# Optimization experiments

Hardware: AMD Instinct MI355X
Metric: run time of the kernel (lower is better)

## Reference

```python
import jax, jax.numpy as jnp
import numpy as np

EMBED_DIM = 1024
NUM_HEADS = 16
HEAD_DIM = EMBED_DIM // NUM_HEADS
INV_SQRT_DIM = 1.0 / np.sqrt(EMBED_DIM).astype(np.float32)  # note: embed_dim, not head_dim


def setup_inputs() -> dict:
    key = jax.random.key(0)
    k1, k2 = jax.random.split(key)
    hidden_states = jax.random.normal(k1, (2, 2048, EMBED_DIM), dtype=jnp.float32)
    # nn.Linear(embed_dim, 3*embed_dim, bias=False); store as [in, out] so y = x @ w_qkv
    w_qkv = jax.random.normal(k2, (EMBED_DIM, 3 * EMBED_DIM), dtype=jnp.float32) * 0.02
    return {"hidden_states": hidden_states, "w_qkv": w_qkv}


def reference(hidden_states, w_qkv):
    b, s, _ = hidden_states.shape
    qkv = hidden_states @ w_qkv  # [b, s, 3*E]
    q, k, v = jnp.split(qkv, 3, axis=-1)

    def split_heads(x):  # [b, s, E] -> [b, h, s, d]
        return x.reshape(b, s, NUM_HEADS, HEAD_DIM).transpose(0, 2, 1, 3)

    q, k, v = split_heads(q), split_heads(k), split_heads(v)
    scores = jnp.einsum('bhqd,bhkd->bhqk', q, k) * INV_SQRT_DIM
    w = jax.nn.softmax(scores, axis=-1)
    out = jnp.einsum('bhqk,bhkd->bhqd', w, v)  # [b, h, s, d]
    return out.transpose(0, 2, 1, 3).reshape(b, s, EMBED_DIM)
```

## Files before the change

### kernel.cpp

```cpp
#include <hip/hip_runtime.h>
#include <stdint.h>


typedef __attribute__((ext_vector_type(8))) short v8s;
typedef __attribute__((ext_vector_type(4))) float v4f;

__device__ __forceinline__ unsigned short bf16bits(float f) {
  union { float f; unsigned int u; } c; c.f = f;
  unsigned int u = c.u;
  unsigned int r = (u + 0x7fffu + ((u >> 16) & 1u)) >> 16;
  return (unsigned short)r;
}

__device__ __forceinline__ v4f mfma16(v8s a, v8s b, v4f c) {
  return __builtin_amdgcn_mfma_f32_16x16x32_bf16(a, b, c, 0, 0, 0);
}

#define GLD16(g, l) __builtin_amdgcn_global_load_lds( \
    (const __attribute__((address_space(1))) unsigned int*)(g), \
    (__attribute__((address_space(3))) unsigned int*)(l), 16, 0, 0)

__global__ __launch_bounds__(256) void cvt_x_kernel(const float4* __restrict__ x4,
                                                    ushort4* __restrict__ o4, int n4) {
  int i = blockIdx.x * 256 + threadIdx.x;
  if (i < n4) {
    float4 v = x4[i];
    ushort4 o;
    o.x = bf16bits(v.x); o.y = bf16bits(v.y); o.z = bf16bits(v.z); o.w = bf16bits(v.w);
    o4[i] = o;
  }
}

__global__ __launch_bounds__(256) void cvt_wT_kernel(const float* __restrict__ w,
                                                     unsigned short* __restrict__ wt) {
  __shared__ float t[32][33];
  int n0 = blockIdx.x * 32, k0 = blockIdx.y * 32;
  int tx = threadIdx.x & 31, ty = threadIdx.x >> 5;
  for (int i = 0; i < 4; ++i) {
    int kr = ty + i * 8;
    t[kr][tx] = w[(k0 + kr) * 3072 + n0 + tx];
  }
  __syncthreads();
  for (int i = 0; i < 4; ++i) {
    int nr = ty + i * 8;
    wt[(n0 + nr) * 1024 + k0 + tx] = bf16bits(t[tx][nr]);
  }
}

__global__ __launch_bounds__(256) void qkv_gemm(const unsigned short* __restrict__ A,
                                                const unsigned short* __restrict__ Bm,
                                                unsigned short* __restrict__ Qh,
                                                unsigned short* __restrict__ Kh,
                                                unsigned short* __restrict__ VTh) {
  __shared__ __align__(16) unsigned short As[128 * 64];
  __shared__ __align__(16) unsigned short Bs[128 * 64];
  int bm = blockIdx.x, bn = blockIdx.y;
  int tid = threadIdx.x, lane = tid & 63, wave = tid >> 6;
  int wr = wave >> 1, wc = wave & 1;

  v4f acc[4][4];
  for (int i = 0; i < 4; ++i)
    for (int j = 0; j < 4; ++j) acc[i][j] = (v4f){0.f, 0.f, 0.f, 0.f};

  for (int kk = 0; kk < 1024; kk += 64) {
    __syncthreads();
    for (int i = 0; i < 4; ++i) {
      int e = i * 256 + tid;
      int row = e >> 3, cc = e & 7;
      int sc = cc ^ (row & 7);
      GLD16(A + (bm * 128 + row) * 1024 + kk + sc * 8,
            (char*)As + (i * 256 + wave * 64) * 16);
    }
    for (int i = 0; i < 4; ++i) {
      int e = i * 256 + tid;
      int row = e >> 3, cc = e & 7;
      int sc = cc ^ (row & 7);
      GLD16(Bm + (bn * 128 + row) * 1024 + kk + sc * 8,
            (char*)Bs + (i * 256 + wave * 64) * 16);
    }
    __syncthreads();
    for (int ks = 0; ks < 2; ++ks) {
      v8s af[4], bf[4];
      for (int rt = 0; rt < 4; ++rt) {
        int ra = wr * 64 + rt * 16 + (lane & 15);
        int ca = (ks * 4 + (lane >> 4)) ^ (ra & 7);
        af[rt] = *(const v8s*)&As[ra * 64 + ca * 8];
      }
      for (int ct = 0; ct < 4; ++ct) {
        int rb = wc * 64 + ct * 16 + (lane & 15);
        int cb = (ks * 4 + (lane >> 4)) ^ (rb & 7);
        bf[ct] = *(const v8s*)&Bs[rb * 64 + cb * 8];
      }
      for (int rt = 0; rt < 4; ++rt)
        for (int ct = 0; ct < 4; ++ct)
          acc[rt][ct] = mfma16(af[rt], bf[ct], acc[rt][ct]);
    }
  }

  int which = (bn * 128) >> 10;
  for (int ct = 0; ct < 4; ++ct) {
    int n = bn * 128 + wc * 64 + ct * 16 + (lane & 15);
    int rem = n & 1023, head = rem >> 6, d = rem & 63;
    for (int rt = 0; rt < 4; ++rt) {
      int m = bm * 128 + wr * 64 + rt * 16 + ((lane >> 4) << 2);
      int b = m >> 11, s = m & 2047;
      int bh = b * 16 + head;
      if (which == 2) {
        ushort4 pk;
        pk.x = bf16bits(acc[rt][ct][0]); pk.y = bf16bits(acc[rt][ct][1]);
        pk.z = bf16bits(acc[rt][ct][2]); pk.w = bf16bits(acc[rt][ct][3]);
        *(ushort4*)&VTh[(bh * 64 + d) * 2048 + s] = pk;
      } else {
        unsigned short* dst = (which == 0 ? Qh : Kh) + (bh * 2048 + s) * 64 + d;
        for (int j = 0; j < 4; ++j) dst[j * 64] = bf16bits(acc[rt][ct][j]);
      }
    }
  }
}

__global__ __launch_bounds__(256) void attn_kernel(const unsigned short* __restrict__ Qh,
                                                   const unsigned short* __restrict__ Kh,
                                                   const unsigned short* __restrict__ VTh,
                                                   float* __restrict__ out) {
  __shared__ __align__(16) unsigned short Qs[64 * 64];
  __shared__ __align__(16) unsigned short Ks[64 * 64];
  __shared__ __align__(16) unsigned short Vs[64 * 64];
  __shared__ __align__(16) unsigned short Ps[64 * 64];
  int qb = blockIdx.x, bh = blockIdx.y;
  int tid = threadIdx.x, lane = tid & 63, wave = tid >> 6;
  int wq = wave * 16;

  const unsigned short* Qg = Qh + (bh * 2048 + qb * 64) * 64;
  const unsigned short* Kg = Kh + bh * 2048 * 64;
  const unsigned short* Vg = VTh + bh * 64 * 2048;

  for (int i = 0; i < 2; ++i) {
    int e = i * 256 + tid;
    int row = e >> 3, cc = e & 7;
    int sc = cc ^ (row & 7);
    GLD16(Qg + row * 64 + sc * 8, (char*)Qs + (i * 256 + wave * 64) * 16);
  }
  __syncthreads();

  v8s qf[2];
  for (int ks = 0; ks < 2; ++ks) {
    int rq = wq + (lane & 15);
    int cq = (ks * 4 + (lane >> 4)) ^ (rq & 7);
    qf[ks] = *(const v8s*)&Qs[rq * 64 + cq * 8];
  }

  v4f oacc[4];
  for (int j = 0; j < 4; ++j) oacc[j] = (v4f){0.f, 0.f, 0.f, 0.f};
  float rsum[4] = {};

  for (int kt = 0; kt < 32; ++kt) {
    __syncthreads();
    for (int i = 0; i < 2; ++i) {
      int e = i * 256 + tid;
      int row = e >> 3, cc = e & 7;
      int sc = cc ^ (row & 7);
      GLD16(Kg + (kt * 64 + row) * 64 + sc * 8, (char*)Ks + (i * 256 + wave * 64) * 16);
    }
    for (int i = 0; i < 2; ++i) {
      int e = i * 256 + tid;
      int row = e >> 3, cc = e & 7;
      int sc = cc ^ (row & 7);
      GLD16(Vg + row * 2048 + kt * 64 + sc * 8, (char*)Vs + (i * 256 + wave * 64) * 16);
    }
    __syncthreads();

    v4f sacc[4];
    for (int j = 0; j < 4; ++j) sacc[j] = (v4f){0.f, 0.f, 0.f, 0.f};
    for (int ks = 0; ks < 2; ++ks) {
      v8s kf[4];
      for (int ct = 0; ct < 4; ++ct) {
        int rk = ct * 16 + (lane & 15);
        int ck = (ks * 4 + (lane >> 4)) ^ (rk & 7);
        kf[ct] = *(const v8s*)&Ks[rk * 64 + ck * 8];
      }
      for (int ct = 0; ct < 4; ++ct)
        sacc[ct] = mfma16(qf[ks], kf[ct], sacc[ct]);
    }

    for (int ct = 0; ct < 4; ++ct)
      for (int j = 0; j < 4; ++j) {
        float p = __expf(sacc[ct][j] * 0.03125f);
        rsum[j] += p;
        int prow = wq + ((lane >> 4) << 2) + j;
        int col = ct * 16 + (lane & 15);
        Ps[prow * 64 + (((col >> 3) ^ (prow & 7)) << 3) + (col & 7)] = bf16bits(p);
      }

    for (int ks4 = 0; ks4 < 2; ++ks4) {
      v8s pa, vb[4];
      int rp = wq + (lane & 15);
      int cp = (ks4 * 4 + (lane >> 4)) ^ (rp & 7);
      pa = *(const v8s*)&Ps[rp * 64 + cp * 8];
      for (int dt = 0; dt < 4; ++dt) {
        int rv = dt * 16 + (lane & 15);
        int cv = (ks4 * 4 + (lane >> 4)) ^ (rv & 7);
        vb[dt] = *(const v8s*)&Vs[rv * 64 + cv * 8];
      }
      for (int dt = 0; dt < 4; ++dt)
        oacc[dt] = mfma16(pa, vb[dt], oacc[dt]);
    }
  }

  for (int j = 0; j < 4; ++j) {
    float v = rsum[j];
    v += __shfl_xor(v, 1, 64);
    v += __shfl_xor(v, 2, 64);
    v += __shfl_xor(v, 4, 64);
    v += __shfl_xor(v, 8, 64);
    rsum[j] = v;
  }

  int b = bh >> 4, h = bh & 15;
  for (int dt = 0; dt < 4; ++dt) {
    int q = qb * 64 + wq + ((lane >> 4) << 2);
    int d = h * 64 + dt * 16 + (lane & 15);
    for (int j = 0; j < 4; ++j)
      out[(b * 2048 + q + j) * 1024 + d] = oacc[dt][j] / rsum[j];
  }
}

extern "C" void kernel_launch(void* const* d_in, const int* in_sizes, int n_in,
                              void* d_out, int out_size, void* d_ws, size_t ws_size,
                              hipStream_t stream) {
  const float* x = (const float*)d_in[0];
  const float* w = (const float*)d_in[1];
  float* out = (float*)d_out;

  char* ws = (char*)d_ws;
  unsigned short* xb = (unsigned short*)ws;
  unsigned short* wT = (unsigned short*)(ws + 8388608);
  unsigned short* Qh = (unsigned short*)(ws + 14680064);
  unsigned short* Kh = (unsigned short*)(ws + 23068672);
  unsigned short* VT = (unsigned short*)(ws + 31457280);

  cvt_x_kernel<<<4096, 256, 0, stream>>>((const float4*)x, (ushort4*)xb, 1048576);
  cvt_wT_kernel<<<dim3(96, 32), 256, 0, stream>>>(w, wT);
  qkv_gemm<<<dim3(32, 24), 256, 0, stream>>>(xb, wT, Qh, Kh, VT);
  attn_kernel<<<dim3(32, 32), 256, 0, stream>>>(Qh, Kh, VT, out);
}
```

Measured before the change: 178.1 us.

## Stage GEMM epilogue through LDS and keep attention P in registers

The QKV GEMM epilogue now writes each tile to shared memory and then emits coalesced 16-byte stores. Q and K go into one row-major [tokens, 2048] buffer, and V is written transposed per head. The attention kernel reads Q and K with a 2048-element stride. It computes S transposed (K as the A operand) so the exp'd probabilities can be packed to bf16 and reshuffled across lanes into the PV MFMA A-operand layout. This removes the Ps shared-memory round trip and its scattered 2-byte stores, and it replaces the per-row divide with a reciprocal-multiply. The cost is extra cross-lane shuffles and selects in the inner loop and strided global reads for Q and K.

```diff
diff --git a/kernel.cpp b/kernel.cpp
--- a/kernel.cpp
+++ b/kernel.cpp
@@ -49,11 +49,11 @@
 
 __global__ __launch_bounds__(256) void qkv_gemm(const unsigned short* __restrict__ A,
                                                 const unsigned short* __restrict__ Bm,
-                                                unsigned short* __restrict__ Qh,
-                                                unsigned short* __restrict__ Kh,
+                                                unsigned short* __restrict__ Cq,
                                                 unsigned short* __restrict__ VTh) {
-  __shared__ __align__(16) unsigned short As[128 * 64];
-  __shared__ __align__(16) unsigned short Bs[128 * 64];
+  __shared__ __align__(16) unsigned short S[128 * 128];
+  unsigned short* As = S;
+  unsigned short* Bs = S + 128 * 64;
   int bm = blockIdx.x, bn = blockIdx.y;
   int tid = threadIdx.x, lane = tid & 63, wave = tid >> 6;
   int wr = wave >> 1, wc = wave & 1;
@@ -97,48 +97,67 @@
     }
   }
 
-  int which = (bn * 128) >> 10;
-  for (int ct = 0; ct < 4; ++ct) {
-    int n = bn * 128 + wc * 64 + ct * 16 + (lane & 15);
-    int rem = n & 1023, head = rem >> 6, d = rem & 63;
-    for (int rt = 0; rt < 4; ++rt) {
-      int m = bm * 128 + wr * 64 + rt * 16 + ((lane >> 4) << 2);
-      int b = m >> 11, s = m & 2047;
-      int bh = b * 16 + head;
-      if (which == 2) {
-        ushort4 pk;
-        pk.x = bf16bits(acc[rt][ct][0]); pk.y = bf16bits(acc[rt][ct][1]);
-        pk.z = bf16bits(acc[rt][ct][2]); pk.w = bf16bits(acc[rt][ct][3]);
-        *(ushort4*)&VTh[(bh * 64 + d) * 2048 + s] = pk;
-      } else {
-        unsigned short* dst = (which == 0 ? Qh : Kh) + (bh * 2048 + s) * 64 + d;
-        for (int j = 0; j < 4; ++j) dst[j * 64] = bf16bits(acc[rt][ct][j]);
-      }
-    }
-  }
-}
-
-__global__ __launch_bounds__(256) void attn_kernel(const unsigned short* __restrict__ Qh,
-                                                   const unsigned short* __restrict__ Kh,
+  __syncthreads();
+  if (bn < 16) {
+    for (int ct = 0; ct < 4; ++ct) {
+      int col = wc * 64 + ct * 16 + (lane & 15);
+      for (int rt = 0; rt < 4; ++rt)
+        for (int j = 0; j < 4; ++j) {
+          int m = wr * 64 + rt * 16 + ((lane >> 4) << 2) + j;
+          S[m * 128 + (((col >> 3) ^ (m & 7)) << 3) + (col & 7)] = bf16bits(acc[rt][ct][j]);
+        }
+    }
+    __syncthreads();
+    for (int i = 0; i < 8; ++i) {
+      int c = i * 256 + tid;
+      int m = c >> 4, c8 = c & 15;
+      v8s v = *(const v8s*)&S[m * 128 + ((c8 ^ (m & 7)) << 3)];
+      *(v8s*)&Cq[(size_t)(bm * 128 + m) * 2048 + bn * 128 + c8 * 8] = v;
+    }
+  } else {
+    for (int ct = 0; ct < 4; ++ct) {
+      int n = wc * 64 + ct * 16 + (lane & 15);
+      for (int rt = 0; rt < 4; ++rt) {
+        int m0 = wr * 64 + rt * 16 + ((lane >> 4) << 2);
+        ushort4 p4;
+        p4.x = bf16bits(acc[rt][ct][0]); p4.y = bf16bits(acc[rt][ct][1]);
+        p4.z = bf16bits(acc[rt][ct][2]); p4.w = bf16bits(acc[rt][ct][3]);
+        *(ushort4*)&S[n * 128 + (((m0 >> 3) ^ (n & 7)) << 3) + (m0 & 7)] = p4;
+      }
+    }
+    __syncthreads();
+    int b = bm >> 4, s0 = (bm & 15) * 128;
+    for (int i = 0; i < 8; ++i) {
+      int c = i * 256 + tid;
+      int n = c >> 4, c8 = c & 15;
+      v8s v = *(const v8s*)&S[n * 128 + ((c8 ^ (n & 7)) << 3)];
+      int nn = bn * 128 + n - 2048;
+      int head = nn >> 6, d = nn & 63;
+      *(v8s*)&VTh[(size_t)((b * 16 + head) * 64 + d) * 2048 + s0 + c8 * 8] = v;
+    }
+  }
+}
+
+__global__ __launch_bounds__(256) void attn_kernel(const unsigned short* __restrict__ Cq,
                                                    const unsigned short* __restrict__ VTh,
                                                    float* __restrict__ out) {
   __shared__ __align__(16) unsigned short Qs[64 * 64];
   __shared__ __align__(16) unsigned short Ks[64 * 64];
   __shared__ __align__(16) unsigned short Vs[64 * 64];
-  __shared__ __align__(16) unsigned short Ps[64 * 64];
   int qb = blockIdx.x, bh = blockIdx.y;
   int tid = threadIdx.x, lane = tid & 63, wave = tid >> 6;
   int wq = wave * 16;
-
-  const unsigned short* Qg = Qh + (bh * 2048 + qb * 64) * 64;
-  const unsigned short* Kg = Kh + bh * 2048 * 64;
-  const unsigned short* Vg = VTh + bh * 64 * 2048;
+  int b = bh >> 4, h = bh & 15;
+
+  const unsigned short* Qg = Cq + (size_t)(b * 2048 + qb * 64) * 2048 + h * 64;
+  const unsigned short* Kg = Cq + (size_t)(b * 2048) * 2048 + 1024 + h * 64;
+  const unsigned short* Vg = VTh + (size_t)bh * 64 * 2048;
 
   for (int i = 0; i < 2; ++i) {
     int e = i * 256 + tid;
     int row = e >> 3, cc = e & 7;
     int sc = cc ^ (row & 7);
-    GLD16(Qg + row * 64 + sc * 8, (char*)Qs + (i * 256 + wave * 64) * 16);
+    GLD16(Qg + (size_t)row * 2048 + sc * 8, (char*)Qs + (i * 256 + wave * 64) * 16);
   }
   __syncthreads();
 
@@ -151,7 +170,11 @@
 
   v4f oacc[4];
   for (int j = 0; j < 4; ++j) oacc[j] = (v4f){0.f, 0.f, 0.f, 0.f};
-  float rsum[4] = {};
+  float rsum = 0.f;
+
+  int sA = (lane & 15) + ((lane & 16) << 1);
+  int sB = sA + 16;
+  bool hi = (lane >= 32);
 
   for (int kt = 0; kt < 32; ++kt) {
     __syncthreads();
@@ -159,7 +182,8 @@
       int e = i * 256 + tid;
       int row = e >> 3, cc = e & 7;
       int sc = cc ^ (row & 7);
-      GLD16(Kg + (kt * 64 + row) * 64 + sc * 8, (char*)Ks + (i * 256 + wave * 64) * 16);
+      GLD16(Kg + (size_t)(kt * 64 + row) * 2048 + sc * 8,
+            (char*)Ks + (i * 256 + wave * 64) * 16);
     }
     for (int i = 0; i < 2; ++i) {
       int e = i * 256 + tid;
@@ -169,8 +193,8 @@
     }
     __syncthreads();
 
-    v4f sacc[4];
-    for (int j = 0; j < 4; ++j) sacc[j] = (v4f){0.f, 0.f, 0.f, 0.f};
+    v4f st[4];
+    for (int j = 0; j < 4; ++j) st[j] = (v4f){0.f, 0.f, 0.f, 0.f};
     for (int ks = 0; ks < 2; ++ks) {
       v8s kf[4];
       for (int ct = 0; ct < 4; ++ct) {
@@ -179,23 +203,44 @@
         kf[ct] = *(const v8s*)&Ks[rk * 64 + ck * 8];
       }
       for (int ct = 0; ct < 4; ++ct)
-        sacc[ct] = mfma16(qf[ks], kf[ct], sacc[ct]);
-    }
-
-    for (int ct = 0; ct < 4; ++ct)
-      for (int j = 0; j < 4; ++j) {
-        float p = __expf(sacc[ct][j] * 0.03125f);
-        rsum[j] += p;
-        int prow = wq + ((lane >> 4) << 2) + j;
-        int col = ct * 16 + (lane & 15);
-        Ps[prow * 64 + (((col >> 3) ^ (prow & 7)) << 3) + (col & 7)] = bf16bits(p);
-      }
-
+        st[ct] = mfma16(kf[ct], qf[ks], st[ct]);
+    }
+
+    unsigned int pk[4][2];
+#pragma unroll
+    for (int ct = 0; ct < 4; ++ct) {
+      float p0 = __expf(st[ct][0] * 0.03125f);
+      float p1 = __expf(st[ct][1] * 0.03125f);
+      float p2 = __expf(st[ct][2] * 0.03125f);
+      float p3 = __expf(st[ct][3] * 0.03125f);
+      rsum += (p0 + p1) + (p2 + p3);
+      pk[ct][0] = (unsigned int)bf16bits(p0) | ((unsigned int)bf16bits(p1) << 16);
+      pk[ct][1] = (unsigned int)bf16bits(p2) | ((unsigned int)bf16bits(p3) << 16);
+    }
+
+    union U { unsigned int u[4]; v8s v; };
+    U u0, u1;
+    {
+      unsigned int a0 = __shfl(pk[0][0], sA, 64), b0 = __shfl(pk[1][0], sA, 64);
+      unsigned int a1 = __shfl(pk[0][1], sA, 64), b1 = __shfl(pk[1][1], sA, 64);
+      unsigned int a2 = __shfl(pk[0][0], sB, 64), b2 = __shfl(pk[1][0], sB, 64);
+      unsigned int a3 = __shfl(pk[0][1], sB, 64), b3 = __shfl(pk[1][1], sB, 64);
+      u0.u[0] = hi ? b0 : a0; u0.u[1] = hi ? b1 : a1;
+      u0.u[2] = hi ? b2 : a2; u0.u[3] = hi ? b3 : a3;
+    }
+    {
+      unsigned int a0 = __shfl(pk[2][0], sA, 64), b0 = __shfl(pk[3][0], sA, 64);
+      unsigned int a1 = __shfl(pk[2][1], sA, 64), b1 = __shfl(pk[3][1], sA, 64);
+      unsigned int a2 = __shfl(pk[2][0], sB, 64), b2 = __shfl(pk[3][0], sB, 64);
+      unsigned int a3 = __shfl(pk[2][1], sB, 64), b3 = __shfl(pk[3][1], sB, 64);
+      u1.u[0] = hi ? b0 : a0; u1.u[1] = hi ? b1 : a1;
+      u1.u[2] = hi ? b2 : a2; u1.u[3] = hi ? b3 : a3;
+    }
+
+#pragma unroll
     for (int ks4 = 0; ks4 < 2; ++ks4) {
-      v8s pa, vb[4];
-      int rp = wq + (lane & 15);
-      int cp = (ks4 * 4 + (lane >> 4)) ^ (rp & 7);
-      pa = *(const v8s*)&Ps[rp * 64 + cp * 8];
+      v8s pa = ks4 ? u1.v : u0.v;
+      v8s vb[4];
       for (int dt = 0; dt < 4; ++dt) {
         int rv = dt * 16 + (lane & 15);
         int cv = (ks4 * 4 + (lane >> 4)) ^ (rv & 7);
@@ -206,21 +251,19 @@
     }
   }
 
-  for (int j = 0; j < 4; ++j) {
-    float v = rsum[j];
-    v += __shfl_xor(v, 1, 64);
-    v += __shfl_xor(v, 2, 64);
-    v += __shfl_xor(v, 4, 64);
-    v += __shfl_xor(v, 8, 64);
-    rsum[j] = v;
-  }
-
-  int b = bh >> 4, h = bh & 15;
+  float rtot = rsum;
+  rtot += __shfl_xor(rtot, 16, 64);
+  rtot += __shfl_xor(rtot, 32, 64);
+  float inv[4];
+#pragma unroll
+  for (int j = 0; j < 4; ++j)
+    inv[j] = 1.f / __shfl(rtot, ((lane >> 4) << 2) + j, 64);
+
   for (int dt = 0; dt < 4; ++dt) {
     int q = qb * 64 + wq + ((lane >> 4) << 2);
     int d = h * 64 + dt * 16 + (lane & 15);
     for (int j = 0; j < 4; ++j)
-      out[(b * 2048 + q + j) * 1024 + d] = oacc[dt][j] / rsum[j];
+      out[(size_t)(b * 2048 + q + j) * 1024 + d] = oacc[dt][j] * inv[j];
   }
 }
 
@@ -234,12 +277,11 @@
   char* ws = (char*)d_ws;
   unsigned short* xb = (unsigned short*)ws;
   unsigned short* wT = (unsigned short*)(ws + 8388608);
-  unsigned short* Qh = (unsigned short*)(ws + 14680064);
-  unsigned short* Kh = (unsigned short*)(ws + 23068672);
+  unsigned short* Cq = (unsigned short*)(ws + 14680064);
   unsigned short* VT = (unsigned short*)(ws + 31457280);
 
   cvt_x_kernel<<<4096, 256, 0, stream>>>((const float4*)x, (ushort4*)xb, 1048576);
   cvt_wT_kernel<<<dim3(96, 32), 256, 0, stream>>>(w, wT);
-  qkv_gemm<<<dim3(32, 24), 256, 0, stream>>>(xb, wT, Qh, Kh, VT);
-  attn_kernel<<<dim3(32, 32), 256, 0, stream>>>(Qh, Kh, VT, out);
-}
+  qkv_gemm<<<dim3(32, 24), 256, 0, stream>>>(xb, wT, Cq, VT);
+  attn_kernel<<<dim3(32, 32), 256, 0, stream>>>(Cq, VT, out);
+}
```

Measured after the change: 190.4 us. 1.07x slower.

## Double-buffer GEMM and attention loads, stage epilogue via LDS, keep Q/K row-major

Applied to the files above, without the earlier changes.

The QKV GEMM now uses 64x128 tiles with a two-stage LDS double buffer, which doubles the grid. Its epilogue stages results through shared memory so Q/K and transposed V can be written with coalesced 16-byte stores. Q and K stay in a row-major [b*s, 2048] buffer that attention reads with a strided layout. Attention double-buffers its K/V tiles, prefetching the next tile while computing the current one. P is now converted to bf16 by truncation instead of round-to-nearest, which adds a small precision bias in exchange for fewer ALU ops.

```diff
diff --git a/kernel.cpp b/kernel.cpp
--- a/kernel.cpp
+++ b/kernel.cpp
@@ -49,26 +49,25 @@
 
 __global__ __launch_bounds__(256) void qkv_gemm(const unsigned short* __restrict__ A,
                                                 const unsigned short* __restrict__ Bm,
-                                                unsigned short* __restrict__ Qh,
-                                                unsigned short* __restrict__ Kh,
+                                                unsigned short* __restrict__ Cq,
                                                 unsigned short* __restrict__ VTh) {
-  __shared__ __align__(16) unsigned short As[128 * 64];
-  __shared__ __align__(16) unsigned short Bs[128 * 64];
+  __shared__ __align__(16) unsigned short S[24576];
   int bm = blockIdx.x, bn = blockIdx.y;
   int tid = threadIdx.x, lane = tid & 63, wave = tid >> 6;
   int wr = wave >> 1, wc = wave & 1;
 
-  v4f acc[4][4];
-  for (int i = 0; i < 4; ++i)
+  v4f acc[2][4];
+  for (int i = 0; i < 2; ++i)
     for (int j = 0; j < 4; ++j) acc[i][j] = (v4f){0.f, 0.f, 0.f, 0.f};
 
-  for (int kk = 0; kk < 1024; kk += 64) {
-    __syncthreads();
-    for (int i = 0; i < 4; ++i) {
+  auto STAGE = [&](int h, int kk) {
+    unsigned short* As = S + h * 12288;
+    unsigned short* Bs = As + 4096;
+    for (int i = 0; i < 2; ++i) {
       int e = i * 256 + tid;
       int row = e >> 3, cc = e & 7;
       int sc = cc ^ (row & 7);
-      GLD16(A + (bm * 128 + row) * 1024 + kk + sc * 8,
+      GLD16(A + (bm * 64 + row) * 1024 + kk + sc * 8,
             (char*)As + (i * 256 + wave * 64) * 16);
     }
     for (int i = 0; i < 4; ++i) {
@@ -78,11 +77,14 @@
       GLD16(Bm + (bn * 128 + row) * 1024 + kk + sc * 8,
             (char*)Bs + (i * 256 + wave * 64) * 16);
     }
-    __syncthreads();
+  };
+  auto COMPUTE = [&](int h) {
+    const unsigned short* As = S + h * 12288;
+    const unsigned short* Bs = As + 4096;
     for (int ks = 0; ks < 2; ++ks) {
-      v8s af[4], bf[4];
-      for (int rt = 0; rt < 4; ++rt) {
-        int ra = wr * 64 + rt * 16 + (lane & 15);
+      v8s af[2], bf[4];
+      for (int rt = 0; rt < 2; ++rt) {
+        int ra = wr * 32 + rt * 16 + (lane & 15);
         int ca = (ks * 4 + (lane >> 4)) ^ (ra & 7);
         af[rt] = *(const v8s*)&As[ra * 64 + ca * 8];
       }
@@ -91,54 +93,85 @@
         int cb = (ks * 4 + (lane >> 4)) ^ (rb & 7);
         bf[ct] = *(const v8s*)&Bs[rb * 64 + cb * 8];
       }
-      for (int rt = 0; rt < 4; ++rt)
+      for (int rt = 0; rt < 2; ++rt)
         for (int ct = 0; ct < 4; ++ct)
           acc[rt][ct] = mfma16(af[rt], bf[ct], acc[rt][ct]);
     }
-  }
-
-  int which = (bn * 128) >> 10;
-  for (int ct = 0; ct < 4; ++ct) {
-    int n = bn * 128 + wc * 64 + ct * 16 + (lane & 15);
-    int rem = n & 1023, head = rem >> 6, d = rem & 63;
-    for (int rt = 0; rt < 4; ++rt) {
-      int m = bm * 128 + wr * 64 + rt * 16 + ((lane >> 4) << 2);
-      int b = m >> 11, s = m & 2047;
-      int bh = b * 16 + head;
-      if (which == 2) {
-        ushort4 pk;
-        pk.x = bf16bits(acc[rt][ct][0]); pk.y = bf16bits(acc[rt][ct][1]);
-        pk.z = bf16bits(acc[rt][ct][2]); pk.w = bf16bits(acc[rt][ct][3]);
-        *(ushort4*)&VTh[(bh * 64 + d) * 2048 + s] = pk;
-      } else {
-        unsigned short* dst = (which == 0 ? Qh : Kh) + (bh * 2048 + s) * 64 + d;
-        for (int j = 0; j < 4; ++j) dst[j * 64] = bf16bits(acc[rt][ct][j]);
-      }
-    }
-  }
-}
-
-__global__ __launch_bounds__(256) void attn_kernel(const unsigned short* __restrict__ Qh,
-                                                   const unsigned short* __restrict__ Kh,
+  };
+
+  STAGE(0, 0);
+  __syncthreads();
+  for (int kt = 0; kt < 15; ++kt) {
+    STAGE((kt + 1) & 1, (kt + 1) * 64);
+    COMPUTE(kt & 1);
+    __syncthreads();
+  }
+  COMPUTE(1);
+  __syncthreads();
+
+  if (bn < 16) {
+    for (int ct = 0; ct < 4; ++ct) {
+      int col = wc * 64 + ct * 16 + (lane & 15);
+      for (int rt = 0; rt < 2; ++rt)
+        for (int j = 0; j < 4; ++j) {
+          int m = wr * 32 + rt * 16 + ((lane >> 4) << 2) + j;
+          S[m * 128 + (((col >> 3) ^ (m & 7)) << 3) + (col & 7)] = bf16bits(acc[rt][ct][j]);
+        }
+    }
+    __syncthreads();
+    for (int i = 0; i < 4; ++i) {
+      int c = i * 256 + tid;
+      int m = c >> 4, c8 = c & 15;
+      v8s v = *(const v8s*)&S[m * 128 + ((c8 ^ (m & 7)) << 3)];
+      *(v8s*)&Cq[(size_t)(bm * 64 + m) * 2048 + bn * 128 + c8 * 8] = v;
+    }
+  } else {
+    for (int ct = 0; ct < 4; ++ct) {
+      int n = wc * 64 + ct * 16 + (lane & 15);
+      for (int rt = 0; rt < 2; ++rt) {
+        int m0 = wr * 32 + rt * 16 + ((lane >> 4) << 2);
+        ushort4 p4;
+        p4.x = bf16bits(acc[rt][ct][0]); p4.y = bf16bits(acc[rt][ct][1]);
+        p4.z = bf16bits(acc[rt][ct][2]); p4.w = bf16bits(acc[rt][ct][3]);
+        *(ushort4*)&S[n * 64 + (((m0 >> 3) ^ (n & 7)) << 3) + (m0 & 7)] = p4;
+      }
+    }
+    __syncthreads();
+    int b = bm >> 5, s0 = (bm & 31) * 64;
+    for (int i = 0; i < 4; ++i) {
+      int c = i * 256 + tid;
+      int n = c >> 3, c8 = c & 7;
+      v8s v = *(const v8s*)&S[n * 64 + ((c8 ^ (n & 7)) << 3)];
+      int nn = bn * 128 + n - 2048;
+      int head = nn >> 6, d = nn & 63;
+      *(v8s*)&VTh[(size_t)((b * 16 + head) * 64 + d) * 2048 + s0 + c8 * 8] = v;
+    }
+  }
+}
+
+__global__ __launch_bounds__(256) void attn_kernel(const unsigned short* __restrict__ Cq,
                                                    const unsigned short* __restrict__ VTh,
                                                    float* __restrict__ out) {
   __shared__ __align__(16) unsigned short Qs[64 * 64];
-  __shared__ __align__(16) unsigned short Ks[64 * 64];
-  __shared__ __align__(16) unsigned short Vs[64 * 64];
+  __shared__ __align__(16) unsigned short Ks[2][64 * 64];
+  __shared__ __align__(16) unsigned short Vs[2][64 * 64];
   __shared__ __align__(16) unsigned short Ps[64 * 64];
   int qb = blockIdx.x, bh = blockIdx.y;
   int tid = threadIdx.x, lane = tid & 63, wave = tid >> 6;
   int wq = wave * 16;
-
-  const unsigned short* Qg = Qh + (bh * 2048 + qb * 64) * 64;
-  const unsigned short* Kg = Kh + bh * 2048 * 64;
-  const unsigned short* Vg = VTh + bh * 64 * 2048;
+  int b = bh >> 4, h = bh & 15;
+
+  const unsigned short* Qg = Cq + (size_t)(b * 2048 + qb * 64) * 2048 + h * 64;
+  const unsigned short* Kg = Cq + (size_t)(b * 2048) * 2048 + 1024 + h * 64;
+  const unsigned short* Vg = VTh + (size_t)bh * 64 * 2048;
 
   for (int i = 0; i < 2; ++i) {
     int e = i * 256 + tid;
     int row = e >> 3, cc = e & 7;
     int sc = cc ^ (row & 7);
-    GLD16(Qg + row * 64 + sc * 8, (char*)Qs + (i * 256 + wave * 64) * 16);
+    GLD16(Qg + (size_t)row * 2048 + sc * 8, (char*)Qs + (i * 256 + wave * 64) * 16);
+    GLD16(Kg + (size_t)row * 2048 + sc * 8, (char*)Ks[0] + (i * 256 + wave * 64) * 16);
+    GLD16(Vg + row * 2048 + sc * 8, (char*)Vs[0] + (i * 256 + wave * 64) * 16);
   }
   __syncthreads();
 
@@ -154,20 +187,18 @@
   float rsum[4] = {};
 
   for (int kt = 0; kt < 32; ++kt) {
-    __syncthreads();
-    for (int i = 0; i < 2; ++i) {
-      int e = i * 256 + tid;
-      int row = e >> 3, cc = e & 7;
-      int sc = cc ^ (row & 7);
-      GLD16(Kg + (kt * 64 + row) * 64 + sc * 8, (char*)Ks + (i * 256 + wave * 64) * 16);
-    }
-    for (int i = 0; i < 2; ++i) {
-      int e = i * 256 + tid;
-      int row = e >> 3, cc = e & 7;
-      int sc = cc ^ (row & 7);
-      GLD16(Vg + row * 2048 + kt * 64 + sc * 8, (char*)Vs + (i * 256 + wave * 64) * 16);
-    }
-    __syncthreads();
+    int cur = kt & 1;
+    if (kt < 31) {
+      for (int i = 0; i < 2; ++i) {
+        int e = i * 256 + tid;
+        int row = e >> 3, cc = e & 7;
+        int sc = cc ^ (row & 7);
+        GLD16(Kg + (size_t)((kt + 1) * 64 + row) * 2048 + sc * 8,
+              (char*)Ks[cur ^ 1] + (i * 256 + wave * 64) * 16);
+        GLD16(Vg + row * 2048 + (kt + 1) * 64 + sc * 8,
+              (char*)Vs[cur ^ 1] + (i * 256 + wave * 64) * 16);
+      }
+    }
 
     v4f sacc[4];
     for (int j = 0; j < 4; ++j) sacc[j] = (v4f){0.f, 0.f, 0.f, 0.f};
@@ -176,7 +207,7 @@
       for (int ct = 0; ct < 4; ++ct) {
         int rk = ct * 16 + (lane & 15);
         int ck = (ks * 4 + (lane >> 4)) ^ (rk & 7);
-        kf[ct] = *(const v8s*)&Ks[rk * 64 + ck * 8];
+        kf[ct] = *(const v8s*)&Ks[cur][rk * 64 + ck * 8];
       }
       for (int ct = 0; ct < 4; ++ct)
         sacc[ct] = mfma16(qf[ks], kf[ct], sacc[ct]);
@@ -186,9 +217,11 @@
       for (int j = 0; j < 4; ++j) {
         float p = __expf(sacc[ct][j] * 0.03125f);
         rsum[j] += p;
+        union { float f; unsigned int u; } cv; cv.f = p;
         int prow = wq + ((lane >> 4) << 2) + j;
         int col = ct * 16 + (lane & 15);
-        Ps[prow * 64 + (((col >> 3) ^ (prow & 7)) << 3) + (col & 7)] = bf16bits(p);
+        Ps[prow * 64 + (((col >> 3) ^ (prow & 7)) << 3) + (col & 7)] =
+            (unsigned short)(cv.u >> 16);
       }
 
     for (int ks4 = 0; ks4 < 2; ++ks4) {
@@ -198,12 +231,13 @@
       pa = *(const v8s*)&Ps[rp * 64 + cp * 8];
       for (int dt = 0; dt < 4; ++dt) {
         int rv = dt * 16 + (lane & 15);
-        int cv = (ks4 * 4 + (lane >> 4)) ^ (rv & 7);
-        vb[dt] = *(const v8s*)&Vs[rv * 64 + cv * 8];
+        int cv2 = (ks4 * 4 + (lane >> 4)) ^ (rv & 7);
+        vb[dt] = *(const v8s*)&Vs[cur][rv * 64 + cv2 * 8];
       }
       for (int dt = 0; dt < 4; ++dt)
         oacc[dt] = mfma16(pa, vb[dt], oacc[dt]);
     }
+    __syncthreads();
   }
 
   for (int j = 0; j < 4; ++j) {
@@ -215,12 +249,11 @@
     rsum[j] = v;
   }
 
-  int b = bh >> 4, h = bh & 15;
   for (int dt = 0; dt < 4; ++dt) {
     int q = qb * 64 + wq + ((lane >> 4) << 2);
     int d = h * 64 + dt * 16 + (lane & 15);
     for (int j = 0; j < 4; ++j)
-      out[(b * 2048 + q + j) * 1024 + d] = oacc[dt][j] / rsum[j];
+      out[(size_t)(b * 2048 + q + j) * 1024 + d] = oacc[dt][j] / rsum[j];
   }
 }
 
@@ -234,12 +267,11 @@
   char* ws = (char*)d_ws;
   unsigned short* xb = (unsigned short*)ws;
   unsigned short* wT = (unsigned short*)(ws + 8388608);
-  unsigned short* Qh = (unsigned short*)(ws + 14680064);
-  unsigned short* Kh = (unsigned short*)(ws + 23068672);
+  unsigned short* Cq = (unsigned short*)(ws + 14680064);
   unsigned short* VT = (unsigned short*)(ws + 31457280);
 
   cvt_x_kernel<<<4096, 256, 0, stream>>>((const float4*)x, (ushort4*)xb, 1048576);
   cvt_wT_kernel<<<dim3(96, 32), 256, 0, stream>>>(w, wT);
-  qkv_gemm<<<dim3(32, 24), 256, 0, stream>>>(xb, wT, Qh, Kh, VT);
-  attn_kernel<<<dim3(32, 32), 256, 0, stream>>>(Qh, Kh, VT, out);
-}
+  qkv_gemm<<<dim3(64, 24), 256, 0, stream>>>(xb, wT, Cq, VT);
+  attn_kernel<<<dim3(32, 32), 256, 0, stream>>>(Cq, VT, out);
+}
```

Measured after the change: 189.6 us. 6.4% more time.
